# Optimization experiments

Measured on AMD Instinct MI355X. Metric: run time of the kernel, lower is better.

Reference implementation:

```python
import jax, jax.numpy as jnp
import numpy as np

B, S, D, H = 2, 2048, 1024, 16
HD = D // H

def setup_inputs() -> dict:
    key = jax.random.key(0)
    ks = jax.random.split(key, 11)
    s = 1.0 / np.sqrt(D)
    return {
        "query": jax.random.normal(ks[0], (B, S, D), jnp.float32),
        "key": jax.random.normal(ks[1], (B, S, D), jnp.float32),
        "value": jax.random.normal(ks[2], (B, S, D), jnp.float32),
        "Wq": jax.random.normal(ks[3], (D, D), jnp.float32) * s,
        "bq": jax.random.normal(ks[4], (D,), jnp.float32) * s,
        "Wk": jax.random.normal(ks[5], (D, D), jnp.float32) * s,
        "bk": jax.random.normal(ks[6], (D,), jnp.float32) * s,
        "Wv": jax.random.normal(ks[7], (D, D), jnp.float32) * s,
        "bv": jax.random.normal(ks[8], (D,), jnp.float32) * s,
        "Wo": jax.random.normal(ks[9], (D, D), jnp.float32) * s,
        "bo": jax.random.normal(ks[10], (D,), jnp.float32) * s,
        "test": 0,
    }

def _heads(x, W, b):
    # [B,S,D] @ [D,D] -> [B,S,D] -> [B,H,S,HD]
    y = x @ W + b
    return y.reshape(B, -1, H, HD).transpose(0, 2, 1, 3)

def reference(query, key, value, Wq, bq, Wk, bk, Wv, bv, Wo, bo, test):
    q = _heads(query, Wq, bq)
    k = _heads(key, Wk, bk)
    v = _heads(value, Wv, bv)
    scale = 1.0 / np.sqrt(HD).astype(np.float32)
    scores = jnp.einsum('bhqd,bhkd->bhqk', q, k) * scale  # [B,H,S,S]
    if test:
        return scores
    prob = jax.nn.softmax(scores, axis=-1)
    out = jnp.einsum('bhqk,bhkd->bhqd', prob, v)
    out = out.transpose(0, 2, 1, 3).reshape(B, -1, D)
    return out @ Wo + bo
```

## Files before the change

kernel.cpp:

```cpp
#include <hip/hip_runtime.h>

constexpr int Bn  = 2;
constexpr int Sn  = 2048;
constexpr int Dn  = 1024;
constexpr int Hn  = 16;
constexpr int HDn = 64;
constexpr int Mn  = Bn * Sn;

typedef _Float16 half8 __attribute__((ext_vector_type(8)));
typedef _Float16 half4 __attribute__((ext_vector_type(4)));
typedef float    f32x4 __attribute__((ext_vector_type(4)));

__device__ __forceinline__ void cp16(const _Float16* g, _Float16* l) {
  __builtin_amdgcn_global_load_lds(
      (__attribute__((address_space(1))) void*)g,
      (__attribute__((address_space(3))) void*)l, 16, 0, 0);
}

__global__ __launch_bounds__(256) void convert_x(
    const float* __restrict__ q, const float* __restrict__ k,
    const float* __restrict__ v, _Float16* __restrict__ Xh) {
  const int z = blockIdx.y;
  const float* src = (z == 0) ? q : (z == 1) ? k : v;
  _Float16* dst = Xh + (size_t)z * (Mn * Dn);
  int i = blockIdx.x * 256 + threadIdx.x;
  float4 v4 = ((const float4*)src)[i];
  half4 h;
  h.x = (_Float16)v4.x; h.y = (_Float16)v4.y;
  h.z = (_Float16)v4.z; h.w = (_Float16)v4.w;
  *(half4*)(dst + (size_t)i * 4) = h;
}

__global__ __launch_bounds__(256) void transpose_w(
    const float* __restrict__ Wq, const float* __restrict__ Wk,
    const float* __restrict__ Wv, const float* __restrict__ Wo,
    _Float16* __restrict__ WT) {
  const int z = blockIdx.z;
  const float* W = (z == 0) ? Wq : (z == 1) ? Wk : (z == 2) ? Wv : Wo;
  _Float16* T = WT + (size_t)z * Dn * Dn;
  __shared__ float tile[64][65];
  const int k0 = blockIdx.y * 64, n0 = blockIdx.x * 64;
  const int tid = threadIdx.x;
#pragma unroll
  for (int i = 0; i < 4; i++) {
    int s = tid + i * 256;
    int r = s >> 4, c4 = s & 15;
    float4 w4 = *(const float4*)(W + (size_t)(k0 + r) * Dn + n0 + c4 * 4);
    tile[r][c4 * 4 + 0] = w4.x; tile[r][c4 * 4 + 1] = w4.y;
    tile[r][c4 * 4 + 2] = w4.z; tile[r][c4 * 4 + 3] = w4.w;
  }
  __syncthreads();
#pragma unroll
  for (int i = 0; i < 2; i++) {
    int s = tid + i * 256;
    int n = s >> 3, r8 = (s & 7) * 8;
    half8 h;
#pragma unroll
    for (int j = 0; j < 8; j++) h[j] = (_Float16)tile[r8 + j][n];
    *(half8*)(T + (size_t)(n0 + n) * Dn + k0 + r8) = h;
  }
}

__global__ __launch_bounds__(256) void proj_kernel(
    const _Float16* __restrict__ Xh, const _Float16* __restrict__ WT,
    const float* __restrict__ bq, const float* __restrict__ bk,
    const float* __restrict__ bv,
    _Float16* __restrict__ Qh, _Float16* __restrict__ Kh,
    _Float16* __restrict__ VT) {
  const int z = blockIdx.z;
  const _Float16* A  = Xh + (size_t)z * Mn * Dn;
  const _Float16* Bm = WT + (size_t)z * Dn * Dn;
  const float* bias = (z == 0) ? bq : (z == 1) ? bk : bv;

  __shared__ __align__(16) _Float16 As[128 * 32];
  __shared__ __align__(16) _Float16 Bs[128 * 32];

  const int tid  = threadIdx.x;
  const int lane = tid & 63;
  const int w    = tid >> 6;
  const int wm   = (w >> 1) * 64;
  const int wn   = (w & 1) * 64;
  const int m0   = blockIdx.y * 128;
  const int n0   = blockIdx.x * 128;
  const int qd   = lane >> 4;
  const int lm   = lane & 15;

  f32x4 acc[4][4];
#pragma unroll
  for (int i = 0; i < 4; i++)
#pragma unroll
    for (int j = 0; j < 4; j++) acc[i][j] = {0.f, 0.f, 0.f, 0.f};

  for (int k0 = 0; k0 < Dn; k0 += 32) {
#pragma unroll
    for (int p = 0; p < 2; p++) {
      int s = tid + p * 256;
      int row = s >> 2, c = s & 3;
      cp16(A + (size_t)(m0 + row) * Dn + k0 + c * 8, As + s * 8);
    }
#pragma unroll
    for (int p = 0; p < 2; p++) {
      int s = tid + p * 256;
      int row = s >> 2, c = s & 3;
      cp16(Bm + (size_t)(n0 + row) * Dn + k0 + c * 8, Bs + s * 8);
    }
    __syncthreads();
    half8 a[4], bb[4];
#pragma unroll
    for (int mi = 0; mi < 4; mi++)
      a[mi] = *(const half8*)(As + (wm + mi * 16 + lm) * 32 + qd * 8);
#pragma unroll
    for (int ni = 0; ni < 4; ni++)
      bb[ni] = *(const half8*)(Bs + (wn + ni * 16 + lm) * 32 + qd * 8);
    if (z < 2) {
#pragma unroll
      for (int mi = 0; mi < 4; mi++)
#pragma unroll
        for (int ni = 0; ni < 4; ni++)
          acc[mi][ni] = __builtin_amdgcn_mfma_f32_16x16x32_f16(bb[ni], a[mi], acc[mi][ni], 0, 0, 0);
    } else {
#pragma unroll
      for (int mi = 0; mi < 4; mi++)
#pragma unroll
        for (int ni = 0; ni < 4; ni++)
          acc[mi][ni] = __builtin_amdgcn_mfma_f32_16x16x32_f16(a[mi], bb[ni], acc[mi][ni], 0, 0, 0);
    }
    __syncthreads();
  }

  if (z < 2) {
    _Float16* out = (z == 0) ? Qh : Kh;
    const float scl = (z == 0) ? 0.125f * 1.44269504089f : 1.0f;
#pragma unroll
    for (int mi = 0; mi < 4; mi++) {
      int m = m0 + wm + mi * 16 + lm;
      int b_ = m >> 11, s_ = m & (Sn - 1);
#pragma unroll
      for (int ni = 0; ni < 4; ni++) {
        int nb = n0 + wn + ni * 16 + qd * 4;
        float4 b4 = *(const float4*)(bias + nb);
        int h = nb >> 6, hd = nb & 63;
        half4 h4;
        h4[0] = (_Float16)((acc[mi][ni][0] + b4.x) * scl);
        h4[1] = (_Float16)((acc[mi][ni][1] + b4.y) * scl);
        h4[2] = (_Float16)((acc[mi][ni][2] + b4.z) * scl);
        h4[3] = (_Float16)((acc[mi][ni][3] + b4.w) * scl);
        *(half4*)(out + (((size_t)(b_ * Hn + h)) * Sn + s_) * HDn + hd) = h4;
      }
    }
  } else {
#pragma unroll
    for (int ni = 0; ni < 4; ni++) {
      int n = n0 + wn + ni * 16 + lm;
      float b_f = bias[n];
      int h = n >> 6, hd = n & 63;
#pragma unroll
      for (int mi = 0; mi < 4; mi++) {
        int mb = m0 + wm + mi * 16 + qd * 4;
        int b_ = mb >> 11, s_ = mb & (Sn - 1);
        half4 h4;
#pragma unroll
        for (int r = 0; r < 4; r++) h4[r] = (_Float16)(acc[mi][ni][r] + b_f);
        *(half4*)(VT + (((size_t)(b_ * Hn + h)) * HDn + hd) * Sn + s_) = h4;
      }
    }
  }
}

__global__ __launch_bounds__(256) void attn_kernel(
    const _Float16* __restrict__ Qh, const _Float16* __restrict__ Kh,
    const _Float16* __restrict__ VT, _Float16* __restrict__ attn_out) {
  constexpr int QK_LD = 72;
  constexpr int PV_LD = 136;
  __shared__ __align__(16) _Float16 smem[128 * QK_LD + 64 * PV_LD + 4 * 32 * PV_LD];
  _Float16* Ks  = smem;
  _Float16* VTs = smem + 128 * QK_LD;
  _Float16* Ps  = VTs + 64 * PV_LD;
  _Float16* Qs  = Ps;

  const int bh = blockIdx.y;
  const int q0 = blockIdx.x * 128;
  const size_t base = (size_t)bh * Sn * HDn;

  const int tid  = threadIdx.x;
  const int lane = tid & 63;
  const int w    = tid >> 6;
  const int qd   = lane >> 4;
  const int lm   = lane & 15;

#pragma unroll
  for (int i = 0; i < 4; i++) {
    int s = tid + i * 256;
    int row = s >> 3, c8 = s & 7;
    *(half8*)(Qs + row * QK_LD + c8 * 8) =
        *(const half8*)(Qh + base + (size_t)(q0 + row) * HDn + c8 * 8);
  }
  __syncthreads();
  half8 qa[2][2];
#pragma unroll
  for (int nj = 0; nj < 2; nj++)
#pragma unroll
    for (int ks = 0; ks < 2; ks++)
      qa[nj][ks] = *(const half8*)(Qs + (w * 32 + nj * 16 + lm) * QK_LD + ks * 32 + qd * 8);

  half8 vones;
#pragma unroll
  for (int j = 0; j < 8; j++) vones[j] = (lm == 0) ? (_Float16)1.0f : (_Float16)0.0f;

  f32x4 oacc[2][4];
#pragma unroll
  for (int i = 0; i < 2; i++)
#pragma unroll
    for (int j = 0; j < 4; j++) oacc[i][j] = {0.f, 0.f, 0.f, 0.f};
  f32x4 oaccl[2] = {{0.f, 0.f, 0.f, 0.f}, {0.f, 0.f, 0.f, 0.f}};

  _Float16* Psw = Ps + w * (32 * PV_LD);
  const f32x4 sinit = {-10.f, -10.f, -10.f, -10.f};

  for (int kt = 0; kt < Sn / 128; kt++) {
    __syncthreads();
    const int kb = kt * 128;
#pragma unroll
    for (int i = 0; i < 4; i++) {
      int s = tid + i * 256;
      int row = s >> 3, c8 = s & 7;
      *(half8*)(Ks + row * QK_LD + c8 * 8) =
          *(const half8*)(Kh + base + (size_t)(kb + row) * HDn + c8 * 8);
    }
#pragma unroll
    for (int i = 0; i < 4; i++) {
      int s = tid + i * 256;
      int hd = s >> 4, c8 = s & 15;
      *(half8*)(VTs + hd * PV_LD + c8 * 8) =
          *(const half8*)(VT + base + (size_t)hd * Sn + kb + c8 * 8);
    }
    __syncthreads();

    f32x4 sacc[8][2];
#pragma unroll
    for (int ni = 0; ni < 8; ni++)
#pragma unroll
      for (int nj = 0; nj < 2; nj++) sacc[ni][nj] = sinit;
#pragma unroll
    for (int ni = 0; ni < 8; ni++)
#pragma unroll
      for (int ks = 0; ks < 2; ks++) {
        half8 ka = *(const half8*)(Ks + (ni * 16 + lm) * QK_LD + ks * 32 + qd * 8);
#pragma unroll
        for (int nj = 0; nj < 2; nj++)
          sacc[ni][nj] = __builtin_amdgcn_mfma_f32_16x16x32_f16(ka, qa[nj][ks], sacc[ni][nj], 0, 0, 0);
      }

#pragma unroll
    for (int nj = 0; nj < 2; nj++)
#pragma unroll
      for (int ni = 0; ni < 8; ni++) {
        float p0 = __builtin_amdgcn_exp2f(sacc[ni][nj][0]);
        float p1 = __builtin_amdgcn_exp2f(sacc[ni][nj][1]);
        float p2 = __builtin_amdgcn_exp2f(sacc[ni][nj][2]);
        float p3 = __builtin_amdgcn_exp2f(sacc[ni][nj][3]);
        auto lo = __builtin_amdgcn_cvt_pkrtz(p0, p1);
        auto hi = __builtin_amdgcn_cvt_pkrtz(p2, p3);
        half4 h4;
        h4[0] = (_Float16)lo[0]; h4[1] = (_Float16)lo[1];
        h4[2] = (_Float16)hi[0]; h4[3] = (_Float16)hi[1];
        *(half4*)(Psw + (nj * 16 + lm) * PV_LD + ni * 16 + qd * 4) = h4;
      }

#pragma unroll
    for (int ks = 0; ks < 4; ks++) {
      half8 pa[2];
#pragma unroll
      for (int mi = 0; mi < 2; mi++)
        pa[mi] = *(const half8*)(Psw + (mi * 16 + lm) * PV_LD + ks * 32 + qd * 8);
#pragma unroll
      for (int oi = 0; oi < 4; oi++) {
        half8 vb = *(const half8*)(VTs + (oi * 16 + lm) * PV_LD + ks * 32 + qd * 8);
#pragma unroll
        for (int mi = 0; mi < 2; mi++)
          oacc[mi][oi] = __builtin_amdgcn_mfma_f32_16x16x32_f16(vb, pa[mi], oacc[mi][oi], 0, 0, 0);
      }
#pragma unroll
      for (int mi = 0; mi < 2; mi++)
        oaccl[mi] = __builtin_amdgcn_mfma_f32_16x16x32_f16(vones, pa[mi], oaccl[mi], 0, 0, 0);
    }
  }

  const int b_ = bh >> 4, h_ = bh & 15;
#pragma unroll
  for (int mi = 0; mi < 2; mi++) {
    float lr = __shfl(oaccl[mi][0], lm, 64);
    float inv = 1.0f / lr;
    int qrow = q0 + w * 32 + mi * 16 + lm;
    size_t rowbase = ((size_t)(b_ * Sn + qrow)) * Dn + h_ * 64;
#pragma unroll
    for (int oi = 0; oi < 4; oi++) {
      half4 h4;
#pragma unroll
      for (int r = 0; r < 4; r++) h4[r] = (_Float16)(oacc[mi][oi][r] * inv);
      *(half4*)(attn_out + rowbase + oi * 16 + qd * 4) = h4;
    }
  }
}

__global__ __launch_bounds__(256) void outproj_kernel(
    const _Float16* __restrict__ Aattn, const _Float16* __restrict__ WoT,
    const float* __restrict__ bo, float* __restrict__ out) {
  __shared__ __align__(16) _Float16 As[128 * 32];
  __shared__ __align__(16) _Float16 Bs[128 * 32];

  const int tid  = threadIdx.x;
  const int lane = tid & 63;
  const int w    = tid >> 6;
  const int wm   = (w >> 1) * 64;
  const int wn   = (w & 1) * 64;
  const int m0   = blockIdx.y * 128;
  const int n0   = blockIdx.x * 128;
  const int qd   = lane >> 4;
  const int lm   = lane & 15;

  f32x4 acc[4][4];
#pragma unroll
  for (int i = 0; i < 4; i++)
#pragma unroll
    for (int j = 0; j < 4; j++) acc[i][j] = {0.f, 0.f, 0.f, 0.f};

  for (int k0 = 0; k0 < Dn; k0 += 32) {
#pragma unroll
    for (int p = 0; p < 2; p++) {
      int s = tid + p * 256;
      int row = s >> 2, c = s & 3;
      cp16(Aattn + (size_t)(m0 + row) * Dn + k0 + c * 8, As + s * 8);
    }
#pragma unroll
    for (int p = 0; p < 2; p++) {
      int s = tid + p * 256;
      int row = s >> 2, c = s & 3;
      cp16(WoT + (size_t)(n0 + row) * Dn + k0 + c * 8, Bs + s * 8);
    }
    __syncthreads();
    half8 a[4], bb[4];
#pragma unroll
    for (int mi = 0; mi < 4; mi++)
      a[mi] = *(const half8*)(As + (wm + mi * 16 + lm) * 32 + qd * 8);
#pragma unroll
    for (int ni = 0; ni < 4; ni++)
      bb[ni] = *(const half8*)(Bs + (wn + ni * 16 + lm) * 32 + qd * 8);
#pragma unroll
    for (int mi = 0; mi < 4; mi++)
#pragma unroll
      for (int ni = 0; ni < 4; ni++)
        acc[mi][ni] = __builtin_amdgcn_mfma_f32_16x16x32_f16(bb[ni], a[mi], acc[mi][ni], 0, 0, 0);
    __syncthreads();
  }
#pragma unroll
  for (int mi = 0; mi < 4; mi++) {
    int m = m0 + wm + mi * 16 + lm;
#pragma unroll
    for (int ni = 0; ni < 4; ni++) {
      int nb = n0 + wn + ni * 16 + qd * 4;
      float4 b4 = *(const float4*)(bo + nb);
      float4 o4;
      o4.x = acc[mi][ni][0] + b4.x;
      o4.y = acc[mi][ni][1] + b4.y;
      o4.z = acc[mi][ni][2] + b4.z;
      o4.w = acc[mi][ni][3] + b4.w;
      *(float4*)(out + (size_t)m * Dn + nb) = o4;
    }
  }
}

extern "C" void kernel_launch(void* const* d_in, const int* in_sizes, int n_in,
                              void* d_out, int out_size, void* d_ws, size_t ws_size,
                              hipStream_t stream) {
  const float* query = (const float*)d_in[0];
  const float* key_  = (const float*)d_in[1];
  const float* value = (const float*)d_in[2];
  const float* Wq = (const float*)d_in[3];
  const float* bq = (const float*)d_in[4];
  const float* Wk = (const float*)d_in[5];
  const float* bk = (const float*)d_in[6];
  const float* Wv = (const float*)d_in[7];
  const float* bv = (const float*)d_in[8];
  const float* Wo = (const float*)d_in[9];
  const float* bo = (const float*)d_in[10];

  _Float16* Xh = (_Float16*)d_ws;
  _Float16* WT = Xh + (size_t)3 * Mn * Dn;
  _Float16* Qh = WT + (size_t)4 * Dn * Dn;
  _Float16* Kh = Qh + (size_t)Mn * Dn;
  _Float16* VT = Kh + (size_t)Mn * Dn;
  _Float16* attnb = Xh;
  float* out = (float*)d_out;

  dim3 blk(256);
  convert_x<<<dim3((Mn * Dn) / (4 * 256), 3), blk, 0, stream>>>(query, key_, value, Xh);
  transpose_w<<<dim3(16, 16, 4), blk, 0, stream>>>(Wq, Wk, Wv, Wo, WT);
  proj_kernel<<<dim3(Dn / 128, Mn / 128, 3), blk, 0, stream>>>(
      Xh, WT, bq, bk, bv, Qh, Kh, VT);
  attn_kernel<<<dim3(Sn / 128, Bn * Hn), blk, 0, stream>>>(Qh, Kh, VT, attnb);
  outproj_kernel<<<dim3(Dn / 128, Mn / 128), blk, 0, stream>>>(
      attnb, WT + (size_t)3 * Dn * Dn, bo, out);
}
```

Measured before the change: 275.1 us.

## Load K and V MFMA operands directly from global memory, dropping LDS staging

The attention kernel no longer stages Q, K and V^T tiles in shared memory with block-wide barriers. Each wave loads its MFMA operands straight from global memory, relying on L1/L2 to serve the four waves that read the same K/V tiles. This removes the LDS copies and both __syncthreads per key tile, and shrinks LDS to just the per-wave P buffer so occupancy can rise. In exchange, global/cache traffic is roughly four times higher and the loads are strided half8 accesses that are not fully coalesced, which exposes memory latency directly to the MFMA chain.

```diff
diff --git a/kernel.cpp b/kernel.cpp
--- a/kernel.cpp
+++ b/kernel.cpp
@@ -170,13 +170,8 @@
 __global__ __launch_bounds__(256) void attn_kernel(
     const _Float16* __restrict__ Qh, const _Float16* __restrict__ Kh,
     const _Float16* __restrict__ VT, _Float16* __restrict__ attn_out) {
-  constexpr int QK_LD = 72;
   constexpr int PV_LD = 136;
-  __shared__ __align__(16) _Float16 smem[128 * QK_LD + 64 * PV_LD + 4 * 32 * PV_LD];
-  _Float16* Ks  = smem;
-  _Float16* VTs = smem + 128 * QK_LD;
-  _Float16* Ps  = VTs + 64 * PV_LD;
-  _Float16* Qs  = Ps;
+  __shared__ __align__(16) _Float16 Ps[4 * 32 * PV_LD];
 
   const int bh = blockIdx.y;
   const int q0 = blockIdx.x * 128;
@@ -188,20 +183,13 @@
   const int qd   = lane >> 4;
   const int lm   = lane & 15;
 
-#pragma unroll
-  for (int i = 0; i < 4; i++) {
-    int s = tid + i * 256;
-    int row = s >> 3, c8 = s & 7;
-    *(half8*)(Qs + row * QK_LD + c8 * 8) =
-        *(const half8*)(Qh + base + (size_t)(q0 + row) * HDn + c8 * 8);
-  }
-  __syncthreads();
+  const _Float16* qptr = Qh + base + (size_t)(q0 + w * 32 + lm) * HDn + qd * 8;
   half8 qa[2][2];
 #pragma unroll
   for (int nj = 0; nj < 2; nj++)
 #pragma unroll
     for (int ks = 0; ks < 2; ks++)
-      qa[nj][ks] = *(const half8*)(Qs + (w * 32 + nj * 16 + lm) * QK_LD + ks * 32 + qd * 8);
+      qa[nj][ks] = *(const half8*)(qptr + nj * 16 * HDn + ks * 32);
 
   half8 vones;
 #pragma unroll
@@ -217,24 +205,18 @@
   _Float16* Psw = Ps + w * (32 * PV_LD);
   const f32x4 sinit = {-10.f, -10.f, -10.f, -10.f};
 
+  const _Float16* kptr = Kh + base + (size_t)lm * HDn + qd * 8;
+  const _Float16* vptr = VT + base + (size_t)lm * Sn + qd * 8;
+
   for (int kt = 0; kt < Sn / 128; kt++) {
-    __syncthreads();
     const int kb = kt * 128;
-#pragma unroll
-    for (int i = 0; i < 4; i++) {
-      int s = tid + i * 256;
-      int row = s >> 3, c8 = s & 7;
-      *(half8*)(Ks + row * QK_LD + c8 * 8) =
-          *(const half8*)(Kh + base + (size_t)(kb + row) * HDn + c8 * 8);
-    }
-#pragma unroll
-    for (int i = 0; i < 4; i++) {
-      int s = tid + i * 256;
-      int hd = s >> 4, c8 = s & 15;
-      *(half8*)(VTs + hd * PV_LD + c8 * 8) =
-          *(const half8*)(VT + base + (size_t)hd * Sn + kb + c8 * 8);
-    }
-    __syncthreads();
+
+    half8 ka[8][2];
+#pragma unroll
+    for (int ni = 0; ni < 8; ni++)
+#pragma unroll
+      for (int ks = 0; ks < 2; ks++)
+        ka[ni][ks] = *(const half8*)(kptr + (size_t)(kb + ni * 16) * HDn + ks * 32);
 
     f32x4 sacc[8][2];
 #pragma unroll
@@ -244,12 +226,10 @@
 #pragma unroll
     for (int ni = 0; ni < 8; ni++)
 #pragma unroll
-      for (int ks = 0; ks < 2; ks++) {
-        half8 ka = *(const half8*)(Ks + (ni * 16 + lm) * QK_LD + ks * 32 + qd * 8);
+      for (int ks = 0; ks < 2; ks++)
 #pragma unroll
         for (int nj = 0; nj < 2; nj++)
-          sacc[ni][nj] = __builtin_amdgcn_mfma_f32_16x16x32_f16(ka, qa[nj][ks], sacc[ni][nj], 0, 0, 0);
-      }
+          sacc[ni][nj] = __builtin_amdgcn_mfma_f32_16x16x32_f16(ka[ni][ks], qa[nj][ks], sacc[ni][nj], 0, 0, 0);
 
 #pragma unroll
     for (int nj = 0; nj < 2; nj++)
@@ -275,7 +255,7 @@
         pa[mi] = *(const half8*)(Psw + (mi * 16 + lm) * PV_LD + ks * 32 + qd * 8);
 #pragma unroll
       for (int oi = 0; oi < 4; oi++) {
-        half8 vb = *(const half8*)(VTs + (oi * 16 + lm) * PV_LD + ks * 32 + qd * 8);
+        half8 vb = *(const half8*)(vptr + (size_t)(oi * 16) * Sn + kb + ks * 32);
 #pragma unroll
         for (int mi = 0; mi < 2; mi++)
           oacc[mi][oi] = __builtin_amdgcn_mfma_f32_16x16x32_f16(vb, pa[mi], oacc[mi][oi], 0, 0, 0);
```

Result: slower. 331.1 us (+20.4%).
